# Performance work log

Hardware: AMD Instinct MI355X
Metric: run time of the kernel (lower is better)

## Reference

```python
import jax, jax.numpy as jnp
import numpy as np

TEMPERATURE = 2.0  # logit_scale buffer
EPS = 1e-8
NEG_FILL = -1e6  # replacement for -inf logits of absent classes


def _l2_normalize(x, eps=EPS):
    # matches torch F.normalize: x / max(||x||, eps)
    n = jnp.sqrt(jnp.sum(x * x, axis=-1, keepdims=True))
    return x / jnp.maximum(n, eps)


def setup_inputs() -> dict:
    key = jax.random.key(0)
    k1, k2, k3 = jax.random.split(key, 3)
    K, M, D, C = 131072, 262144, 128, 256
    return {
        "support_feats": jax.random.normal(k1, (K, D), dtype=jnp.float32),
        "support_labels": jax.random.randint(k2, (K,), 0, C),
        "query_feats": jax.random.normal(k3, (M, D), dtype=jnp.float32),
        "num_classes": C,
    }


def reference(support_feats, support_labels, query_feats, num_classes):
    # Identity projection (in_dim == proj_dim, learnable=False)
    s = _l2_normalize(support_feats)            # [K, D]
    q = _l2_normalize(query_feats)              # [M, D]

    # per-class prototype means via segment-sum (replaces python class loop)
    ones = jnp.ones(s.shape[0], dtype=s.dtype)
    counts = jax.ops.segment_sum(ones, support_labels, num_segments=num_classes)   # [C]
    sums = jax.ops.segment_sum(s, support_labels, num_segments=num_classes)        # [C, D]
    protos = sums / jnp.maximum(counts, 1.0)[:, None]                              # [C, D]

    # -||q - p||^2 = 2 q.p - ||q||^2 - ||p||^2 (single batched GEMM)
    q_sq = jnp.sum(q * q, axis=-1, keepdims=True)        # [M, 1]
    p_sq = jnp.sum(protos * protos, axis=-1)             # [C]
    sims = 2.0 * (q @ protos.T) - q_sq - p_sq[None, :]   # [M, C]

    logits = sims * jnp.float32(TEMPERATURE)
    # absent classes were -inf; after scaling they are replaced by -1e6
    present = counts > 0
    logits = jnp.where(present[None, :], logits, jnp.float32(NEG_FILL))
    return logits
```

## Files before the change

kernel.cpp:

```cpp
#include <hip/hip_runtime.h>
#include <hip/hip_bf16.h>


#define NCLS 256
#define DIM  128

typedef _Float16 f16x8 __attribute__((ext_vector_type(8)));
typedef _Float16 f16x4 __attribute__((ext_vector_type(4)));
typedef float    f32x4 __attribute__((ext_vector_type(4)));

__global__ __launch_bounds__(1024) void proto_partial_kernel(
    const float* __restrict__ sf, const int* __restrict__ lab,
    float* __restrict__ part, int K, int nblocks)
{
    __shared__ float acc[NCLS * DIM];
    __shared__ float cnt[NCLS];

    for (int i = threadIdx.x; i < NCLS * DIM; i += 1024) acc[i] = 0.0f;
    if (threadIdx.x < NCLS) cnt[threadIdx.x] = 0.0f;
    __syncthreads();

    const int lane = threadIdx.x & 63;
    const int wid  = (blockIdx.x * 1024 + threadIdx.x) >> 6;
    const int nw   = (nblocks * 1024) >> 6;

    for (int row = wid; row < K; row += nw) {
        float x0 = __builtin_nontemporal_load(&sf[(size_t)row * DIM + lane]);
        float x1 = __builtin_nontemporal_load(&sf[(size_t)row * DIM + 64 + lane]);
        float ss = x0 * x0 + x1 * x1;
        #pragma unroll
        for (int off = 32; off > 0; off >>= 1) ss += __shfl_xor(ss, off, 64);
        float rn = 1.0f / fmaxf(sqrtf(ss), 1e-8f);
        int c = lab[row];
        atomicAdd(&acc[c * DIM + lane],      x0 * rn);
        atomicAdd(&acc[c * DIM + 64 + lane], x1 * rn);
        if (lane == 0) atomicAdd(&cnt[c], 1.0f);
    }
    __syncthreads();

    float* slot = part + (size_t)blockIdx.x * (NCLS * DIM + NCLS);
    for (int i = threadIdx.x; i < NCLS * DIM; i += 1024) slot[i] = acc[i];
    if (threadIdx.x < NCLS) slot[NCLS * DIM + threadIdx.x] = cnt[threadIdx.x];
}

__global__ __launch_bounds__(128) void proto_reduce_kernel(
    const float* __restrict__ part, int nb,
    float* __restrict__ psq, float* __restrict__ pcnt,
    _Float16* __restrict__ pbh, _Float16* __restrict__ pbl)
{
    const int c = blockIdx.x;
    const int d = threadIdx.x;
    const size_t slot = (size_t)(NCLS * DIM + NCLS);

    float s = 0.0f;
    for (int b = 0; b < nb; ++b) s += part[(size_t)b * slot + c * DIM + d];
    float cn = 0.0f;
    for (int b = 0; b < nb; ++b) cn += part[(size_t)b * slot + NCLS * DIM + c];

    float p = s / fmaxf(cn, 1.0f);

    _Float16 ph = (_Float16)p;
    _Float16 pl = (_Float16)(p - (float)ph);
    int fi = (((c >> 4) * 4 + (d >> 5)) * 64 + ((d >> 3) & 3) * 16 + (c & 15)) * 8 + (d & 7);
    pbh[fi] = ph;
    pbl[fi] = pl;

    float pp = p * p;
    #pragma unroll
    for (int off = 32; off > 0; off >>= 1) pp += __shfl_xor(pp, off, 64);
    __shared__ float tmp[2];
    if ((threadIdx.x & 63) == 0) tmp[threadIdx.x >> 6] = pp;
    __syncthreads();
    if (threadIdx.x == 0) { psq[c] = tmp[0] + tmp[1]; pcnt[c] = cn; }
}

#define BM 64

__global__ __launch_bounds__(512, 4) void logits_mfma_kernel(
    const float* __restrict__ q,
    const float* __restrict__ psq, const float* __restrict__ pcnt,
    const _Float16* __restrict__ pbh, const _Float16* __restrict__ pbl,
    float* __restrict__ out)
{
    __shared__ char  qh_l[BM * 256];
    __shared__ char  ql_l[BM * 256];
    __shared__ float qsq_l[BM];
    __shared__ float psq_l[NCLS];
    __shared__ float pcnt_l[NCLS];

    const int tid  = threadIdx.x;
    const int lane = tid & 63;
    const int wid  = tid >> 6;
    const int wr   = wid >> 2;
    const int wc   = wid & 3;
    const int row0 = blockIdx.x * BM;

    #pragma unroll
    for (int it = 0; it < BM / 16; ++it) {
        const int row = it * 16 + (tid >> 5);
        const int cf  = (tid & 31) * 4;
        f32x4 v = __builtin_nontemporal_load(
            reinterpret_cast<const f32x4*>(&q[(size_t)(row0 + row) * DIM + cf]));

        float ss = v[0] * v[0] + v[1] * v[1] + v[2] * v[2] + v[3] * v[3];
        #pragma unroll
        for (int m = 16; m > 0; m >>= 1) ss += __shfl_xor(ss, m, 64);
        if ((tid & 31) == 0) qsq_l[row] = ss;

        _Float16 h0 = (_Float16)v[0], h1 = (_Float16)v[1],
                 h2 = (_Float16)v[2], h3 = (_Float16)v[3];
        f16x4 h4 = {h0, h1, h2, h3};
        f16x4 l4 = {(_Float16)(v[0] - (float)h0), (_Float16)(v[1] - (float)h1),
                    (_Float16)(v[2] - (float)h2), (_Float16)(v[3] - (float)h3)};
        uint32_t b = (uint32_t)(row * 256 + cf * 2) ^ (uint32_t)((row & 7) << 4);
        *reinterpret_cast<f16x4*>(qh_l + b) = h4;
        *reinterpret_cast<f16x4*>(ql_l + b) = l4;
    }
    if (tid < NCLS) { psq_l[tid] = psq[tid]; pcnt_l[tid] = pcnt[tid]; }
    __syncthreads();

    f32x4 zero = {0.f, 0.f, 0.f, 0.f};
    f32x4 acc[2][4];
    #pragma unroll
    for (int i = 0; i < 2; ++i)
        #pragma unroll
        for (int j = 0; j < 4; ++j) acc[i][j] = zero;

    for (int kk = 0; kk < 4; ++kk) {
        f16x8 ah[2], al[2];
        const int k0 = kk * 32 + (lane >> 4) * 8;
        #pragma unroll
        for (int i = 0; i < 2; ++i) {
            const int row = wr * 32 + i * 16 + (lane & 15);
            uint32_t b = (uint32_t)(row * 256 + k0 * 2) ^ (uint32_t)((row & 7) << 4);
            ah[i] = *reinterpret_cast<const f16x8*>(qh_l + b);
            al[i] = *reinterpret_cast<const f16x8*>(ql_l + b);
        }
        #pragma unroll
        for (int j = 0; j < 4; ++j) {
            const int ct = wc * 4 + j;
            f16x8 bh = *reinterpret_cast<const f16x8*>(pbh + ((ct * 4 + kk) * 64 + lane) * 8);
            f16x8 bl = *reinterpret_cast<const f16x8*>(pbl + ((ct * 4 + kk) * 64 + lane) * 8);
            #pragma unroll
            for (int i = 0; i < 2; ++i) {
                acc[i][j] = __builtin_amdgcn_mfma_f32_16x16x32_f16(ah[i], bh, acc[i][j], 0, 0, 0);
                acc[i][j] = __builtin_amdgcn_mfma_f32_16x16x32_f16(al[i], bh, acc[i][j], 0, 0, 0);
                acc[i][j] = __builtin_amdgcn_mfma_f32_16x16x32_f16(ah[i], bl, acc[i][j], 0, 0, 0);
            }
        }
    }

    float rnv[2][4], qn2v[2][4];
    #pragma unroll
    for (int i = 0; i < 2; ++i)
        #pragma unroll
        for (int r = 0; r < 4; ++r) {
            const int rowl = wr * 32 + i * 16 + (lane >> 4) * 4 + r;
            float ss = qsq_l[rowl];
            float rn = 1.0f / fmaxf(sqrtf(ss), 1e-8f);
            rnv[i][r]  = rn;
            qn2v[i][r] = ss * rn * rn;
        }
    #pragma unroll
    for (int j = 0; j < 4; ++j) {
        const int col = wc * 64 + j * 16 + (lane & 15);
        const float pq = psq_l[col];
        const bool  pr = pcnt_l[col] > 0.5f;
        #pragma unroll
        for (int i = 0; i < 2; ++i) {
            #pragma unroll
            for (int r = 0; r < 4; ++r) {
                const int rowl = wr * 32 + i * 16 + (lane >> 4) * 4 + r;
                float v = 2.0f * (2.0f * acc[i][j][r] * rnv[i][r] - qn2v[i][r] - pq);
                __builtin_nontemporal_store(pr ? v : -1e6f,
                    &out[(size_t)(row0 + rowl) * NCLS + col]);
            }
        }
    }
}

extern "C" void kernel_launch(void* const* d_in, const int* in_sizes, int n_in,
                              void* d_out, int out_size, void* d_ws, size_t ws_size,
                              hipStream_t stream)
{
    const float* sf  = (const float*)d_in[0];
    const int*   lab = (const int*)d_in[1];
    const float* qf  = (const float*)d_in[2];
    float*       out = (float*)d_out;

    const int K = in_sizes[0] / DIM;
    const int M = in_sizes[2] / DIM;

    char* ws = (char*)d_ws;
    float*    psq  = (float*)(ws);
    float*    pcnt = (float*)(ws + 1024);
    _Float16* pbh  = (_Float16*)(ws + 2048);
    _Float16* pbl  = (_Float16*)(ws + 67584);
    float*    part = (float*)(ws + 133120);

    const size_t base_bytes = 133120;
    const size_t slot_bytes = (size_t)(NCLS * DIM + NCLS) * sizeof(float);
    int nb1 = 1;
    if (ws_size > base_bytes + slot_bytes) {
        size_t n = (ws_size - base_bytes) / slot_bytes;
        nb1 = (int)(n < 256 ? n : 256);
        if (nb1 < 1) nb1 = 1;
    }

    proto_partial_kernel<<<nb1, 1024, 0, stream>>>(sf, lab, part, K, nb1);
    proto_reduce_kernel<<<NCLS, 128, 0, stream>>>(part, nb1, psq, pcnt, pbh, pbl);
    logits_mfma_kernel<<<M / BM, 512, 0, stream>>>(qf, psq, pcnt, pbh, pbl, out);
}
```

Before: 639.9 us.

## Swap MFMA operands for vectorized 16-byte output stores; parallelize count reduction

```diff
diff --git a/kernel.cpp b/kernel.cpp
--- a/kernel.cpp
+++ b/kernel.cpp
@@ -52,10 +52,25 @@
     const int d = threadIdx.x;
     const size_t slot = (size_t)(NCLS * DIM + NCLS);
 
-    float s = 0.0f;
-    for (int b = 0; b < nb; ++b) s += part[(size_t)b * slot + c * DIM + d];
-    float cn = 0.0f;
-    for (int b = 0; b < nb; ++b) cn += part[(size_t)b * slot + NCLS * DIM + c];
+    float s0 = 0.0f, s1 = 0.0f, s2 = 0.0f, s3 = 0.0f;
+    int b = 0;
+    for (; b + 3 < nb; b += 4) {
+        s0 += part[(size_t)(b + 0) * slot + c * DIM + d];
+        s1 += part[(size_t)(b + 1) * slot + c * DIM + d];
+        s2 += part[(size_t)(b + 2) * slot + c * DIM + d];
+        s3 += part[(size_t)(b + 3) * slot + c * DIM + d];
+    }
+    for (; b < nb; ++b) s0 += part[(size_t)b * slot + c * DIM + d];
+    float s = (s0 + s1) + (s2 + s3);
+
+    float cnp = 0.0f;
+    for (int bb = d; bb < nb; bb += 128) cnp += part[(size_t)bb * slot + NCLS * DIM + c];
+    #pragma unroll
+    for (int off = 32; off > 0; off >>= 1) cnp += __shfl_xor(cnp, off, 64);
+    __shared__ float cn_l[2];
+    if ((d & 63) == 0) cn_l[d >> 6] = cnp;
+    __syncthreads();
+    const float cn = cn_l[0] + cn_l[1];
 
     float p = s / fmaxf(cn, 1.0f);
 
@@ -69,9 +84,9 @@
     #pragma unroll
     for (int off = 32; off > 0; off >>= 1) pp += __shfl_xor(pp, off, 64);
     __shared__ float tmp[2];
-    if ((threadIdx.x & 63) == 0) tmp[threadIdx.x >> 6] = pp;
-    __syncthreads();
-    if (threadIdx.x == 0) { psq[c] = tmp[0] + tmp[1]; pcnt[c] = cn; }
+    if ((d & 63) == 0) tmp[d >> 6] = pp;
+    __syncthreads();
+    if (d == 0) { psq[c] = tmp[0] + tmp[1]; pcnt[c] = cn; }
 }
 
 #define BM 64
@@ -112,69 +127,61 @@
         f16x4 h4 = {h0, h1, h2, h3};
         f16x4 l4 = {(_Float16)(v[0] - (float)h0), (_Float16)(v[1] - (float)h1),
                     (_Float16)(v[2] - (float)h2), (_Float16)(v[3] - (float)h3)};
-        uint32_t b = (uint32_t)(row * 256 + cf * 2) ^ (uint32_t)((row & 7) << 4);
-        *reinterpret_cast<f16x4*>(qh_l + b) = h4;
-        *reinterpret_cast<f16x4*>(ql_l + b) = l4;
+        uint32_t bofs = (uint32_t)(row * 256 + cf * 2) ^ (uint32_t)((row & 7) << 4);
+        *reinterpret_cast<f16x4*>(qh_l + bofs) = h4;
+        *reinterpret_cast<f16x4*>(ql_l + bofs) = l4;
     }
     if (tid < NCLS) { psq_l[tid] = psq[tid]; pcnt_l[tid] = pcnt[tid]; }
     __syncthreads();
 
     f32x4 zero = {0.f, 0.f, 0.f, 0.f};
-    f32x4 acc[2][4];
-    #pragma unroll
-    for (int i = 0; i < 2; ++i)
-        #pragma unroll
-        for (int j = 0; j < 4; ++j) acc[i][j] = zero;
+    f32x4 acc[4][2];
+    #pragma unroll
+    for (int j = 0; j < 4; ++j)
+        #pragma unroll
+        for (int i = 0; i < 2; ++i) acc[j][i] = zero;
 
     for (int kk = 0; kk < 4; ++kk) {
-        f16x8 ah[2], al[2];
+        f16x8 qbh[2], qbl[2];
         const int k0 = kk * 32 + (lane >> 4) * 8;
         #pragma unroll
         for (int i = 0; i < 2; ++i) {
             const int row = wr * 32 + i * 16 + (lane & 15);
-            uint32_t b = (uint32_t)(row * 256 + k0 * 2) ^ (uint32_t)((row & 7) << 4);
-            ah[i] = *reinterpret_cast<const f16x8*>(qh_l + b);
-            al[i] = *reinterpret_cast<const f16x8*>(ql_l + b);
+            uint32_t bofs = (uint32_t)(row * 256 + k0 * 2) ^ (uint32_t)((row & 7) << 4);
+            qbh[i] = *reinterpret_cast<const f16x8*>(qh_l + bofs);
+            qbl[i] = *reinterpret_cast<const f16x8*>(ql_l + bofs);
         }
         #pragma unroll
         for (int j = 0; j < 4; ++j) {
             const int ct = wc * 4 + j;
-            f16x8 bh = *reinterpret_cast<const f16x8*>(pbh + ((ct * 4 + kk) * 64 + lane) * 8);
-            f16x8 bl = *reinterpret_cast<const f16x8*>(pbl + ((ct * 4 + kk) * 64 + lane) * 8);
+            f16x8 pah = *reinterpret_cast<const f16x8*>(pbh + ((ct * 4 + kk) * 64 + lane) * 8);
+            f16x8 pal = *reinterpret_cast<const f16x8*>(pbl + ((ct * 4 + kk) * 64 + lane) * 8);
             #pragma unroll
             for (int i = 0; i < 2; ++i) {
-                acc[i][j] = __builtin_amdgcn_mfma_f32_16x16x32_f16(ah[i], bh, acc[i][j], 0, 0, 0);
-                acc[i][j] = __builtin_amdgcn_mfma_f32_16x16x32_f16(al[i], bh, acc[i][j], 0, 0, 0);
-                acc[i][j] = __builtin_amdgcn_mfma_f32_16x16x32_f16(ah[i], bl, acc[i][j], 0, 0, 0);
+                acc[j][i] = __builtin_amdgcn_mfma_f32_16x16x32_f16(pah, qbh[i], acc[j][i], 0, 0, 0);
+                acc[j][i] = __builtin_amdgcn_mfma_f32_16x16x32_f16(pah, qbl[i], acc[j][i], 0, 0, 0);
+                acc[j][i] = __builtin_amdgcn_mfma_f32_16x16x32_f16(pal, qbh[i], acc[j][i], 0, 0, 0);
             }
         }
     }
 
-    float rnv[2][4], qn2v[2][4];
-    #pragma unroll
-    for (int i = 0; i < 2; ++i)
-        #pragma unroll
-        for (int r = 0; r < 4; ++r) {
-            const int rowl = wr * 32 + i * 16 + (lane >> 4) * 4 + r;
-            float ss = qsq_l[rowl];
-            float rn = 1.0f / fmaxf(sqrtf(ss), 1e-8f);
-            rnv[i][r]  = rn;
-            qn2v[i][r] = ss * rn * rn;
-        }
-    #pragma unroll
-    for (int j = 0; j < 4; ++j) {
-        const int col = wc * 64 + j * 16 + (lane & 15);
-        const float pq = psq_l[col];
-        const bool  pr = pcnt_l[col] > 0.5f;
-        #pragma unroll
-        for (int i = 0; i < 2; ++i) {
+    #pragma unroll
+    for (int i = 0; i < 2; ++i) {
+        const int qrow = wr * 32 + i * 16 + (lane & 15);
+        const float ss = qsq_l[qrow];
+        const float rn = 1.0f / fmaxf(sqrtf(ss), 1e-8f);
+        const float qn2 = ss * rn * rn;
+        #pragma unroll
+        for (int j = 0; j < 4; ++j) {
+            const int cb = wc * 64 + j * 16 + (lane >> 4) * 4;
+            float tmp4[4];
             #pragma unroll
             for (int r = 0; r < 4; ++r) {
-                const int rowl = wr * 32 + i * 16 + (lane >> 4) * 4 + r;
-                float v = 2.0f * (2.0f * acc[i][j][r] * rnv[i][r] - qn2v[i][r] - pq);
-                __builtin_nontemporal_store(pr ? v : -1e6f,
-                    &out[(size_t)(row0 + rowl) * NCLS + col]);
+                float v = 2.0f * (2.0f * acc[j][i][r] * rn - qn2 - psq_l[cb + r]);
+                tmp4[r] = (pcnt_l[cb + r] > 0.5f) ? v : -1e6f;
             }
+            __builtin_nontemporal_store(*reinterpret_cast<const f32x4*>(tmp4),
+                reinterpret_cast<f32x4*>(&out[(size_t)(row0 + qrow) * NCLS + cb]));
         }
     }
 }
```

After: 540.8 us. -15.5%, faster.
